# Optimization experiments

Hardware: AMD Instinct MI355X
Metric: run time of the kernel (lower is better)

The kernel has to match this reference:

```python
import jax, jax.numpy as jnp
import numpy as np

N_WIN, P, C = 2048, 64, 256      # total windows, tokens per window (8x8 partition), channels
M_SEL, KEEP, REAL = 1536, 48, 40 # selected windows, topk tokens kept per window, real (non-padded)
H, DH = 8, 32                    # heads, dim_head
EPS = 1e-5


def _ln(x, g, b):
    mu = jnp.mean(x, axis=-1, keepdims=True)
    v = jnp.mean(jnp.square(x - mu), axis=-1, keepdims=True)
    return (x - mu) * jax.lax.rsqrt(v + EPS) * g + b


def setup_inputs() -> dict:
    key = jax.random.key(0)
    ks = jax.random.split(key, 6)
    rng = np.random.default_rng(0)
    # distinct selected windows
    index_window = jnp.asarray(np.sort(rng.choice(N_WIN, size=M_SEL, replace=False)), jnp.int32)
    # per selected window: 48 distinct token positions out of 64; first 40 real, last 8 padded
    pos = np.argsort(rng.random((M_SEL, P)), axis=1)[:, :KEEP]
    tok = np.arange(M_SEL)[:, None] * P + pos           # flat rows into (M*P, C)
    index_token = jnp.asarray(tok.reshape(-1), jnp.int32)
    asy_index = jnp.asarray(tok[:, :REAL].reshape(-1), jnp.int32)
    padding_index = jnp.asarray(tok[:, REAL:].reshape(-1), jnp.int32)
    w = lambda k, s: jax.random.normal(k, s, jnp.float32) * 0.02
    return {
        "x": jax.random.normal(ks[0], (N_WIN, P, C), jnp.float32),
        "qkv_w": w(ks[1], (C, 3 * C)), "qkv_b": jnp.zeros((3 * C,), jnp.float32),
        "proj_w": w(ks[2], (C, C)), "proj_b": jnp.zeros((C,), jnp.float32),
        "norm1_g": jnp.ones((C,), jnp.float32), "norm1_b": jnp.zeros((C,), jnp.float32),
        "norm2_g": jnp.ones((C,), jnp.float32), "norm2_b": jnp.zeros((C,), jnp.float32),
        "ls1_g": jnp.full((C,), 1e-5, jnp.float32), "ls2_g": jnp.full((C,), 1e-5, jnp.float32),
        "mlp_w1": w(ks[3], (C, 4 * C)), "mlp_b1": jnp.zeros((4 * C,), jnp.float32),
        "mlp_w2": w(ks[4], (4 * C, C)), "mlp_b2": jnp.zeros((C,), jnp.float32),
        "index_window": index_window, "index_token": index_token,
        "padding_index": padding_index, "asy_index": asy_index,
        "M": M_SEL,
    }


def reference(x, qkv_w, qkv_b, proj_w, proj_b, norm1_g, norm1_b, norm2_g, norm2_b,
              ls1_g, ls2_g, mlp_w1, mlp_b1, mlp_w2, mlp_b2,
              index_window, index_token, padding_index, asy_index, M):
    scale = DH ** -0.5
    x1 = _ln(x, norm1_g, norm1_b)                       # norm1 over all windows (N,P,C)
    X = x1
    XX = x1[index_window].reshape(-1, C)                # gather selected windows -> (M*P, C)
    XX = XX.at[asy_index].set(_ln(XX[asy_index], norm2_g, norm2_b))
    shortcut = XX[asy_index]
    xt = XX[index_token].reshape(M, KEEP, C)            # gather kept tokens per window
    qkv = (xt @ qkv_w + qkv_b).reshape(M, KEEP, H, 3 * DH).transpose(0, 2, 1, 3)
    q, k, v = jnp.split(qkv, 3, axis=-1)                # each (M,H,KEEP,DH)
    attn = jnp.einsum('mhqd,mhkd->mhqk', q, k) * scale  # (M,H,Q,K)
    # scatter scores into full map keyed by KEY token row, mask padded keys, gather back
    am = attn.transpose(0, 3, 2, 1).reshape(M * KEEP, KEEP, H)
    attn_map = jnp.zeros((M * P, KEEP, H), attn.dtype)
    attn_map = attn_map.at[index_token].set(am)
    attn_map = attn_map.at[padding_index].set(-10000.0)
    attn = attn_map[index_token].reshape(M, KEEP, KEEP, H).transpose(0, 3, 2, 1)
    attn = jax.nn.softmax(attn, axis=-1)
    out = jnp.einsum('mhqk,mhkd->mhqd', attn, v).transpose(0, 2, 1, 3).reshape(M, KEEP, C)
    out = out @ proj_w + proj_b
    XX = XX.at[index_token].set(out.reshape(-1, C))
    xa = shortcut + XX[asy_index] * ls1_g               # residual + LayerScale
    hdn = jax.nn.gelu(xa @ mlp_w1 + mlp_b1, approximate=False)
    xa = xa + (hdn @ mlp_w2 + mlp_b2) * ls2_g           # (enable_CB=False path)
    XX = XX.at[asy_index].set(xa)
    Xw = X[index_window].reshape(-1, C)
    XX = XX.at[padding_index].set(Xw[padding_index])    # restore padded rows
    X = X.at[index_window].set(XX.reshape(M, P, C))     # scatter windows back
    return X
```

## Files before the change

### kernel.cpp

```cpp
#include <hip/hip_runtime.h>

typedef __attribute__((ext_vector_type(8))) short bf16x8;
typedef __attribute__((ext_vector_type(4))) float f32x4;
typedef unsigned short u16;
typedef unsigned int u32;

#define NWIN 2048
#define P 64
#define C 256
#define MSEL 1536
#define KEEP 48
#define REAL 40
#define H 8
#define DH 32
#define MROWS (MSEL * REAL)

#define OFF_WQKVT  0
#define OFF_PROJT  196608
#define OFF_W1T    262144
#define OFF_W2T    524288
#define OFF_A      786432
#define OFF_QKV    16515072
#define OFF_ATTNO  63700992
#define OFF_XA     79429632
#define OFF_H      16515072

__device__ __forceinline__ u16 f2bf(float f) {
    u32 u = __float_as_uint(f);
    u += 0x7FFF + ((u >> 16) & 1);
    return (u16)(u >> 16);
}
__device__ __forceinline__ float bf2f(u16 h) { return __uint_as_float(((u32)h) << 16); }

__global__ __launch_bounds__(256) void prep_weights(const float* __restrict__ qkv_w,
                                                    const float* __restrict__ proj_w,
                                                    const float* __restrict__ w1,
                                                    const float* __restrict__ w2,
                                                    u16* __restrict__ ws) {
    int i = blockIdx.x * 256 + threadIdx.x;
    float v; int o;
    if (i < 196608) {
        int n = i >> 8, k = i & 255; v = qkv_w[k * 768 + n]; o = OFF_WQKVT + i;
    } else if (i < 262144) {
        int j = i - 196608; int n = j >> 8, k = j & 255; v = proj_w[k * 256 + n]; o = i;
    } else if (i < 524288) {
        int j = i - 262144; int n = j >> 8, k = j & 255; v = w1[k * 1024 + n]; o = i;
    } else {
        int j = i - 524288; int n = j >> 10, k = j & 1023; v = w2[k * 256 + n]; o = i;
    }
    ws[o] = f2bf(v);
}

__global__ __launch_bounds__(256) void ln1_kernel(const float* __restrict__ x,
                                                  const float* __restrict__ g,
                                                  const float* __restrict__ b,
                                                  float* __restrict__ out) {
    int row = blockIdx.x * 4 + (threadIdx.x >> 6);
    int l = threadIdx.x & 63;
    const float4 v = *(const float4*)(x + (size_t)row * C + l * 4);
    float s = v.x + v.y + v.z + v.w;
    float q = v.x * v.x + v.y * v.y + v.z * v.z + v.w * v.w;
    #pragma unroll
    for (int m = 1; m < 64; m <<= 1) { s += __shfl_xor(s, m); q += __shfl_xor(q, m); }
    float mu = s * (1.0f / C);
    float var = q * (1.0f / C) - mu * mu;
    float rs = rsqrtf(var + 1e-5f);
    float4 gg = *(const float4*)(g + l * 4);
    float4 bb = *(const float4*)(b + l * 4);
    float4 o;
    o.x = (v.x - mu) * rs * gg.x + bb.x;
    o.y = (v.y - mu) * rs * gg.y + bb.y;
    o.z = (v.z - mu) * rs * gg.z + bb.z;
    o.w = (v.w - mu) * rs * gg.w + bb.w;
    *(float4*)(out + (size_t)row * C + l * 4) = o;
}

__global__ __launch_bounds__(256) void ln2_kernel(const float* __restrict__ ln1,
                                                  const float* __restrict__ g,
                                                  const float* __restrict__ b,
                                                  const int* __restrict__ asy,
                                                  const int* __restrict__ iwin,
                                                  u16* __restrict__ A) {
    int r = blockIdx.x * 4 + (threadIdx.x >> 6);
    int l = threadIdx.x & 63;
    int flat = asy[r];
    int m = flat >> 6, p = flat & 63;
    int w = iwin[m];
    const float4 v = *(const float4*)(ln1 + ((size_t)w * P + p) * C + l * 4);
    float s = v.x + v.y + v.z + v.w;
    float q = v.x * v.x + v.y * v.y + v.z * v.z + v.w * v.w;
    #pragma unroll
    for (int mm = 1; mm < 64; mm <<= 1) { s += __shfl_xor(s, mm); q += __shfl_xor(q, mm); }
    float mu = s * (1.0f / C);
    float var = q * (1.0f / C) - mu * mu;
    float rs = rsqrtf(var + 1e-5f);
    float4 gg = *(const float4*)(g + l * 4);
    float4 bb = *(const float4*)(b + l * 4);
    ushort4 o;
    o.x = f2bf((v.x - mu) * rs * gg.x + bb.x);
    o.y = f2bf((v.y - mu) * rs * gg.y + bb.y);
    o.z = f2bf((v.z - mu) * rs * gg.z + bb.z);
    o.w = f2bf((v.w - mu) * rs * gg.w + bb.w);
    *(ushort4*)(A + (size_t)r * C + l * 4) = o;
}

template <int N, int K, class Epi>
__global__ __launch_bounds__(256) void gemm_bt(const u16* __restrict__ A,
                                               const u16* __restrict__ B, Epi epi,
                                               int chunk) {
    constexpr int NB = N / 128;
    int bid = blockIdx.x;
    bid = (bid & 7) * chunk + (bid >> 3);
    int bm = bid / NB, bn = bid % NB;
    __shared__ u16 lA[128 * 64], lB[128 * 64];
    int t = threadIdx.x;
    int l = t & 63, w = t >> 6;
    int wr = w >> 1, wc = w & 1;
    int l15 = l & 15, g4 = l >> 4;
    int xr = l15 & 7;

    f32x4 acc[4][4];
    #pragma unroll
    for (int a = 0; a < 4; a++)
        #pragma unroll
        for (int bb = 0; bb < 4; bb++)
            #pragma unroll
            for (int i = 0; i < 4; i++) acc[a][bb][i] = 0.0f;

    int rbase = w * 32 + (l >> 3);
    int cg = (l & 7) ^ (l >> 3);
    const u16* gA = A + (size_t)(bm * 128 + rbase) * K + cg * 8;
    const u16* gB = B + (size_t)(bn * 128 + rbase) * K + cg * 8;

    for (int k0 = 0; k0 < K; k0 += 64) {
        __syncthreads();
        #pragma unroll
        for (int j = 0; j < 4; j++)
            __builtin_amdgcn_global_load_lds(
                (const __attribute__((address_space(1))) u32*)(gA + (size_t)j * 8 * K + k0),
                (__attribute__((address_space(3))) u32*)(lA + w * 2048 + j * 512), 16, 0, 0);
        #pragma unroll
        for (int j = 0; j < 4; j++)
            __builtin_amdgcn_global_load_lds(
                (const __attribute__((address_space(1))) u32*)(gB + (size_t)j * 8 * K + k0),
                (__attribute__((address_space(3))) u32*)(lB + w * 2048 + j * 512), 16, 0, 0);
        __syncthreads();
        #pragma unroll
        for (int kk = 0; kk < 2; kk++) {
            bf16x8 af[4], bfr[4];
            #pragma unroll
            for (int mt = 0; mt < 4; mt++)
                af[mt] = *(const bf16x8*)(lA + (wr * 64 + mt * 16 + l15) * 64
                                             + ((kk * 4 + g4) ^ xr) * 8);
            #pragma unroll
            for (int nt = 0; nt < 4; nt++)
                bfr[nt] = *(const bf16x8*)(lB + (wc * 64 + nt * 16 + l15) * 64
                                              + ((kk * 4 + g4) ^ xr) * 8);
            #pragma unroll
            for (int mt = 0; mt < 4; mt++)
                #pragma unroll
                for (int nt = 0; nt < 4; nt++)
                    acc[mt][nt] = __builtin_amdgcn_mfma_f32_16x16x32_bf16(af[mt], bfr[nt], acc[mt][nt], 0, 0, 0);
        }
    }
    int orow = bm * 128 + wr * 64, ocol = bn * 128 + wc * 64;
    #pragma unroll
    for (int mt = 0; mt < 4; mt++)
        #pragma unroll
        for (int nt = 0; nt < 4; nt++)
            #pragma unroll
            for (int rg = 0; rg < 4; rg++)
                epi(orow + mt * 16 + g4 * 4 + rg, ocol + nt * 16 + l15, acc[mt][nt][rg]);
}

struct EpiQKV {
    const float* bias; u16* out;
    __device__ void operator()(int r, int c, float v) const {
        out[(size_t)r * 768 + c] = f2bf(v + bias[c]);
    }
};
struct EpiProj {
    const float* bias; const float* ls1; const u16* Abuf; u16* xa;
    __device__ void operator()(int r, int c, float v) const {
        float val = bf2f(Abuf[(size_t)r * 256 + c]) + (v + bias[c]) * ls1[c];
        xa[(size_t)r * 256 + c] = f2bf(val);
    }
};
struct EpiMLP1 {
    const float* bias; u16* h;
    __device__ void operator()(int r, int c, float v) const {
        float x = v + bias[c];
        float gl = 0.5f * x * (1.0f + erff(x * 0.70710678118654752f));
        h[(size_t)r * 1024 + c] = f2bf(gl);
    }
};
struct EpiMLP2 {
    const float* bias; const float* ls2; const u16* xa;
    const int* asy; const int* iwin; float* out;
    __device__ void operator()(int r, int c, float v) const {
        float val = bf2f(xa[(size_t)r * 256 + c]) + (v + bias[c]) * ls2[c];
        int flat = asy[r];
        int m = flat >> 6, p = flat & 63;
        int wdw = iwin[m];
        out[((size_t)wdw * P + p) * C + c] = val;
    }
};

__global__ __launch_bounds__(256) void attn_kernel(const u16* __restrict__ QKV,
                                                   u16* __restrict__ out) {
    __shared__ u16 lds[4 * (48 * 80 + 32 * 80)];
    int m = blockIdx.x;
    int t = threadIdx.x, l = t & 63, w = t >> 6;
    int l15 = l & 15, g4 = l >> 4;
    u16* Pb = lds + w * (48 * 80 + 32 * 80);
    u16* Vt = Pb + 48 * 80;

    u32* z = (u32*)Pb;
    for (int i = l; i < (48 * 80 + 32 * 80) / 2; i += 64) z[i] = 0;

    const float scale = 0.17677669529663687f;

    for (int hh = 0; hh < 2; hh++) {
        int h = w + hh * 4;
        const u16* base = QKV + (size_t)m * REAL * 768 + h * 96;

        for (int i = l; i < REAL * 4; i += 64) {
            int kk = i >> 2, dg = i & 3;
            bf16x8 vv = *(const bf16x8*)(base + (size_t)kk * 768 + 64 + dg * 8);
            #pragma unroll
            for (int j = 0; j < 8; j++) Vt[(dg * 8 + j) * 80 + kk] = vv[j];
        }

        bf16x8 zf;
        #pragma unroll
        for (int i = 0; i < 8; i++) zf[i] = 0;
        bf16x8 qf[3], kf[3];
        #pragma unroll
        for (int mt = 0; mt < 3; mt++) {
            int q = mt * 16 + l15;
            qf[mt] = (q < REAL) ? *(const bf16x8*)(base + (size_t)q * 768 + g4 * 8) : zf;
        }
        #pragma unroll
        for (int nt = 0; nt < 3; nt++) {
            int kk = nt * 16 + l15;
            kf[nt] = (kk < REAL) ? *(const bf16x8*)(base + (size_t)kk * 768 + 32 + g4 * 8) : zf;
        }
        f32x4 s[3][3];
        #pragma unroll
        for (int a = 0; a < 3; a++)
            #pragma unroll
            for (int bb = 0; bb < 3; bb++)
                #pragma unroll
                for (int i = 0; i < 4; i++) s[a][bb][i] = 0.0f;
        #pragma unroll
        for (int mt = 0; mt < 3; mt++)
            #pragma unroll
            for (int nt = 0; nt < 3; nt++)
                s[mt][nt] = __builtin_amdgcn_mfma_f32_16x16x32_bf16(qf[mt], kf[nt], s[mt][nt], 0, 0, 0);

        #pragma unroll
        for (int mt = 0; mt < 3; mt++) {
            #pragma unroll
            for (int rg = 0; rg < 4; rg++) {
                float v0 = s[mt][0][rg] * scale;
                float v1 = s[mt][1][rg] * scale;
                float v2 = s[mt][2][rg] * scale;
                bool k2ok = (32 + l15) < REAL;
                float mx = fmaxf(fmaxf(v0, v1), k2ok ? v2 : -1e30f);
                #pragma unroll
                for (int xm = 1; xm < 16; xm <<= 1) mx = fmaxf(mx, __shfl_xor(mx, xm));
                float e0 = __expf(v0 - mx);
                float e1 = __expf(v1 - mx);
                float e2 = k2ok ? __expf(v2 - mx) : 0.0f;
                float sm = e0 + e1 + e2;
                #pragma unroll
                for (int xm = 1; xm < 16; xm <<= 1) sm += __shfl_xor(sm, xm);
                float inv = 1.0f / sm;
                int q = mt * 16 + g4 * 4 + rg;
                Pb[q * 80 + l15]      = f2bf(e0 * inv);
                Pb[q * 80 + 16 + l15] = f2bf(e1 * inv);
                Pb[q * 80 + 32 + l15] = f2bf(e2 * inv);
            }
        }

        f32x4 o[3][2];
        #pragma unroll
        for (int a = 0; a < 3; a++)
            #pragma unroll
            for (int bb = 0; bb < 2; bb++)
                #pragma unroll
                for (int i = 0; i < 4; i++) o[a][bb][i] = 0.0f;
        #pragma unroll
        for (int kt = 0; kt < 2; kt++) {
            bf16x8 pf[3], vf[2];
            #pragma unroll
            for (int mt = 0; mt < 3; mt++)
                pf[mt] = *(const bf16x8*)(Pb + (mt * 16 + l15) * 80 + kt * 32 + g4 * 8);
            #pragma unroll
            for (int nt = 0; nt < 2; nt++)
                vf[nt] = *(const bf16x8*)(Vt + (nt * 16 + l15) * 80 + kt * 32 + g4 * 8);
            #pragma unroll
            for (int mt = 0; mt < 3; mt++)
                #pragma unroll
                for (int nt = 0; nt < 2; nt++)
                    o[mt][nt] = __builtin_amdgcn_mfma_f32_16x16x32_bf16(pf[mt], vf[nt], o[mt][nt], 0, 0, 0);
        }
        #pragma unroll
        for (int mt = 0; mt < 3; mt++)
            #pragma unroll
            for (int nt = 0; nt < 2; nt++)
                #pragma unroll
                for (int rg = 0; rg < 4; rg++) {
                    int q = mt * 16 + g4 * 4 + rg;
                    if (q < REAL)
                        out[((size_t)m * REAL + q) * C + h * DH + nt * 16 + l15] = f2bf(o[mt][nt][rg]);
                }
    }
}

extern "C" void kernel_launch(void* const* d_in, const int* in_sizes, int n_in,
                              void* d_out, int out_size, void* d_ws, size_t ws_size,
                              hipStream_t stream) {
    const float* x      = (const float*)d_in[0];
    const float* qkv_w  = (const float*)d_in[1];
    const float* qkv_b  = (const float*)d_in[2];
    const float* proj_w = (const float*)d_in[3];
    const float* proj_b = (const float*)d_in[4];
    const float* n1g    = (const float*)d_in[5];
    const float* n1b    = (const float*)d_in[6];
    const float* n2g    = (const float*)d_in[7];
    const float* n2b    = (const float*)d_in[8];
    const float* ls1    = (const float*)d_in[9];
    const float* ls2    = (const float*)d_in[10];
    const float* w1     = (const float*)d_in[11];
    const float* b1     = (const float*)d_in[12];
    const float* w2     = (const float*)d_in[13];
    const float* b2     = (const float*)d_in[14];
    const int*   iwin   = (const int*)d_in[15];
    const int*   asy    = (const int*)d_in[18];
    float* out = (float*)d_out;
    u16* ws = (u16*)d_ws;

    u16* WqkvT = ws + OFF_WQKVT;
    u16* ProjT = ws + OFF_PROJT;
    u16* W1T   = ws + OFF_W1T;
    u16* W2T   = ws + OFF_W2T;
    u16* Abuf  = ws + OFF_A;
    u16* QKV   = ws + OFF_QKV;
    u16* AttnO = ws + OFF_ATTNO;
    u16* XA    = ws + OFF_XA;
    u16* Hbuf  = ws + OFF_H;

    prep_weights<<<3072, 256, 0, stream>>>(qkv_w, proj_w, w1, w2, ws);
    ln1_kernel<<<(NWIN * P) / 4, 256, 0, stream>>>(x, n1g, n1b, out);
    ln2_kernel<<<MROWS / 4, 256, 0, stream>>>(out, n2g, n2b, asy, iwin, Abuf);
    {
        int nwg = (MROWS / 128) * 6;
        gemm_bt<768, 256, EpiQKV><<<nwg, 256, 0, stream>>>(Abuf, WqkvT, EpiQKV{qkv_b, QKV}, nwg / 8);
    }
    attn_kernel<<<MSEL, 256, 0, stream>>>(QKV, AttnO);
    {
        int nwg = (MROWS / 128) * 2;
        gemm_bt<256, 256, EpiProj><<<nwg, 256, 0, stream>>>(AttnO, ProjT, EpiProj{proj_b, ls1, Abuf, XA}, nwg / 8);
    }
    {
        int nwg = (MROWS / 128) * 8;
        gemm_bt<1024, 256, EpiMLP1><<<nwg, 256, 0, stream>>>(XA, W1T, EpiMLP1{b1, Hbuf}, nwg / 8);
    }
    {
        int nwg = (MROWS / 128) * 2;
        gemm_bt<256, 1024, EpiMLP2><<<nwg, 256, 0, stream>>>(Hbuf, W2T, EpiMLP2{b2, ls2, XA, asy, iwin, out}, nwg / 8);
    }
}
```

Baseline: 517.7 us.

## Fuse proj, MLP1 with GELU, and MLP2 into one per-row-tile kernel

Replaces the three separate GEMM launches (projection, MLP up with GELU, MLP down) with one kernel that processes 64 rows per block. The projection output and the hidden activations stay in LDS, chunked 128 hidden columns at a time, so the XA and H intermediates never go to global memory. In exchange the weight B-fragments are read straight from global/L2 with no LDS staging or pipelining. The proj and MLP2 output tiles are smaller (64 rows) than the tuned 128x128 GEMM tiles, which may hurt MFMA efficiency.

```diff
diff --git a/kernel.cpp b/kernel.cpp
--- a/kernel.cpp
+++ b/kernel.cpp
@@ -22,8 +22,6 @@
 #define OFF_A      786432
 #define OFF_QKV    16515072
 #define OFF_ATTNO  63700992
-#define OFF_XA     79429632
-#define OFF_H      16515072
 
 __device__ __forceinline__ u16 f2bf(float f) {
     u32 u = __float_as_uint(f);
@@ -179,32 +177,6 @@
         out[(size_t)r * 768 + c] = f2bf(v + bias[c]);
     }
 };
-struct EpiProj {
-    const float* bias; const float* ls1; const u16* Abuf; u16* xa;
-    __device__ void operator()(int r, int c, float v) const {
-        float val = bf2f(Abuf[(size_t)r * 256 + c]) + (v + bias[c]) * ls1[c];
-        xa[(size_t)r * 256 + c] = f2bf(val);
-    }
-};
-struct EpiMLP1 {
-    const float* bias; u16* h;
-    __device__ void operator()(int r, int c, float v) const {
-        float x = v + bias[c];
-        float gl = 0.5f * x * (1.0f + erff(x * 0.70710678118654752f));
-        h[(size_t)r * 1024 + c] = f2bf(gl);
-    }
-};
-struct EpiMLP2 {
-    const float* bias; const float* ls2; const u16* xa;
-    const int* asy; const int* iwin; float* out;
-    __device__ void operator()(int r, int c, float v) const {
-        float val = bf2f(xa[(size_t)r * 256 + c]) + (v + bias[c]) * ls2[c];
-        int flat = asy[r];
-        int m = flat >> 6, p = flat & 63;
-        int wdw = iwin[m];
-        out[((size_t)wdw * P + p) * C + c] = val;
-    }
-};
 
 __global__ __launch_bounds__(256) void attn_kernel(const u16* __restrict__ QKV,
                                                    u16* __restrict__ out) {
@@ -316,6 +288,150 @@
                         out[((size_t)m * REAL + q) * C + h * DH + nt * 16 + l15] = f2bf(o[mt][nt][rg]);
                 }
     }
+}
+
+__global__ __launch_bounds__(256) void fused_tail(const u16* __restrict__ AttnO,
+                                                  const u16* __restrict__ Abuf,
+                                                  const u16* __restrict__ ProjT,
+                                                  const u16* __restrict__ W1T,
+                                                  const u16* __restrict__ W2T,
+                                                  const float* __restrict__ proj_b,
+                                                  const float* __restrict__ ls1,
+                                                  const float* __restrict__ b1,
+                                                  const float* __restrict__ b2,
+                                                  const float* __restrict__ ls2,
+                                                  const int* __restrict__ asy,
+                                                  const int* __restrict__ iwin,
+                                                  float* __restrict__ out) {
+    __shared__ u16 Xs[64 * 264];
+    __shared__ u16 Hs[64 * 136];
+    int r0 = blockIdx.x * 64;
+    int t = threadIdx.x, l = t & 63, w = t >> 6;
+    int l15 = l & 15, g4 = l >> 4;
+
+    #pragma unroll
+    for (int i = 0; i < 8; i++) {
+        int flat = i * 2048 + t * 8;
+        int row = flat >> 8, col = flat & 255;
+        bf16x8 v = *(const bf16x8*)(AttnO + (size_t)(r0 + row) * 256 + col);
+        *(bf16x8*)(Xs + row * 264 + col) = v;
+    }
+    __syncthreads();
+
+    f32x4 accp[4][4];
+    #pragma unroll
+    for (int a = 0; a < 4; a++)
+        #pragma unroll
+        for (int bb = 0; bb < 4; bb++)
+            #pragma unroll
+            for (int i = 0; i < 4; i++) accp[a][bb][i] = 0.0f;
+    for (int k0 = 0; k0 < 256; k0 += 32) {
+        bf16x8 af[4], bf[4];
+        #pragma unroll
+        for (int mt = 0; mt < 4; mt++)
+            af[mt] = *(const bf16x8*)(Xs + (mt * 16 + l15) * 264 + k0 + g4 * 8);
+        #pragma unroll
+        for (int nt = 0; nt < 4; nt++)
+            bf[nt] = *(const bf16x8*)(ProjT + (size_t)(w * 64 + nt * 16 + l15) * 256 + k0 + g4 * 8);
+        #pragma unroll
+        for (int mt = 0; mt < 4; mt++)
+            #pragma unroll
+            for (int nt = 0; nt < 4; nt++)
+                accp[mt][nt] = __builtin_amdgcn_mfma_f32_16x16x32_bf16(af[mt], bf[nt], accp[mt][nt], 0, 0, 0);
+    }
+    __syncthreads();
+
+    #pragma unroll
+    for (int nt = 0; nt < 4; nt++) {
+        int col = w * 64 + nt * 16 + l15;
+        float pb = proj_b[col], l1 = ls1[col];
+        #pragma unroll
+        for (int mt = 0; mt < 4; mt++)
+            #pragma unroll
+            for (int rg = 0; rg < 4; rg++) {
+                int row = mt * 16 + g4 * 4 + rg;
+                float xa = bf2f(Abuf[(size_t)(r0 + row) * 256 + col]) + (accp[mt][nt][rg] + pb) * l1;
+                Xs[row * 264 + col] = f2bf(xa);
+            }
+    }
+    __syncthreads();
+
+    f32x4 acco[4][4];
+    #pragma unroll
+    for (int a = 0; a < 4; a++)
+        #pragma unroll
+        for (int bb = 0; bb < 4; bb++)
+            #pragma unroll
+            for (int i = 0; i < 4; i++) acco[a][bb][i] = 0.0f;
+
+    for (int kc = 0; kc < 8; kc++) {
+        f32x4 acch[4][2];
+        #pragma unroll
+        for (int a = 0; a < 4; a++)
+            #pragma unroll
+            for (int bb = 0; bb < 2; bb++)
+                #pragma unroll
+                for (int i = 0; i < 4; i++) acch[a][bb][i] = 0.0f;
+        for (int k0 = 0; k0 < 256; k0 += 32) {
+            bf16x8 af[4], bf[2];
+            #pragma unroll
+            for (int mt = 0; mt < 4; mt++)
+                af[mt] = *(const bf16x8*)(Xs + (mt * 16 + l15) * 264 + k0 + g4 * 8);
+            #pragma unroll
+            for (int nt = 0; nt < 2; nt++)
+                bf[nt] = *(const bf16x8*)(W1T + (size_t)(kc * 128 + w * 32 + nt * 16 + l15) * 256 + k0 + g4 * 8);
+            #pragma unroll
+            for (int mt = 0; mt < 4; mt++)
+                #pragma unroll
+                for (int nt = 0; nt < 2; nt++)
+                    acch[mt][nt] = __builtin_amdgcn_mfma_f32_16x16x32_bf16(af[mt], bf[nt], acch[mt][nt], 0, 0, 0);
+        }
+        __syncthreads();
+        #pragma unroll
+        for (int nt = 0; nt < 2; nt++) {
+            int col = w * 32 + nt * 16 + l15;
+            float bb1 = b1[kc * 128 + col];
+            #pragma unroll
+            for (int mt = 0; mt < 4; mt++)
+                #pragma unroll
+                for (int rg = 0; rg < 4; rg++) {
+                    int row = mt * 16 + g4 * 4 + rg;
+                    float x = acch[mt][nt][rg] + bb1;
+                    float gl = 0.5f * x * (1.0f + erff(x * 0.70710678118654752f));
+                    Hs[row * 136 + col] = f2bf(gl);
+                }
+        }
+        __syncthreads();
+        for (int k0 = 0; k0 < 128; k0 += 32) {
+            bf16x8 af[4], bf[4];
+            #pragma unroll
+            for (int mt = 0; mt < 4; mt++)
+                af[mt] = *(const bf16x8*)(Hs + (mt * 16 + l15) * 136 + k0 + g4 * 8);
+            #pragma unroll
+            for (int nt = 0; nt < 4; nt++)
+                bf[nt] = *(const bf16x8*)(W2T + (size_t)(w * 64 + nt * 16 + l15) * 1024 + kc * 128 + k0 + g4 * 8);
+            #pragma unroll
+            for (int mt = 0; mt < 4; mt++)
+                #pragma unroll
+                for (int nt = 0; nt < 4; nt++)
+                    acco[mt][nt] = __builtin_amdgcn_mfma_f32_16x16x32_bf16(af[mt], bf[nt], acco[mt][nt], 0, 0, 0);
+        }
+    }
+
+    #pragma unroll
+    for (int mt = 0; mt < 4; mt++)
+        #pragma unroll
+        for (int rg = 0; rg < 4; rg++) {
+            int row = mt * 16 + g4 * 4 + rg;
+            int flat = asy[r0 + row];
+            size_t orow = ((size_t)iwin[flat >> 6] * P + (flat & 63)) * C;
+            #pragma unroll
+            for (int nt = 0; nt < 4; nt++) {
+                int col = w * 64 + nt * 16 + l15;
+                float xa = bf2f(Xs[row * 264 + col]);
+                out[orow + col] = xa + (acco[mt][nt][rg] + b2[col]) * ls2[col];
+            }
+        }
 }
 
 extern "C" void kernel_launch(void* const* d_in, const int* in_sizes, int n_in,
@@ -348,8 +464,6 @@
     u16* Abuf  = ws + OFF_A;
     u16* QKV   = ws + OFF_QKV;
     u16* AttnO = ws + OFF_ATTNO;
-    u16* XA    = ws + OFF_XA;
-    u16* Hbuf  = ws + OFF_H;
 
     prep_weights<<<3072, 256, 0, stream>>>(qkv_w, proj_w, w1, w2, ws);
     ln1_kernel<<<(NWIN * P) / 4, 256, 0, stream>>>(x, n1g, n1b, out);
@@ -359,16 +473,6 @@
         gemm_bt<768, 256, EpiQKV><<<nwg, 256, 0, stream>>>(Abuf, WqkvT, EpiQKV{qkv_b, QKV}, nwg / 8);
     }
     attn_kernel<<<MSEL, 256, 0, stream>>>(QKV, AttnO);
-    {
-        int nwg = (MROWS / 128) * 2;
-        gemm_bt<256, 256, EpiProj><<<nwg, 256, 0, stream>>>(AttnO, ProjT, EpiProj{proj_b, ls1, Abuf, XA}, nwg / 8);
-    }
-    {
-        int nwg = (MROWS / 128) * 8;
-        gemm_bt<1024, 256, EpiMLP1><<<nwg, 256, 0, stream>>>(XA, W1T, EpiMLP1{b1, Hbuf}, nwg / 8);
-    }
-    {
-        int nwg = (MROWS / 128) * 2;
-        gemm_bt<256, 1024, EpiMLP2><<<nwg, 256, 0, stream>>>(Hbuf, W2T, EpiMLP2{b2, ls2, XA, asy, iwin, out}, nwg / 8);
-    }
-}
+    fused_tail<<<MROWS / 64, 256, 0, stream>>>(AttnO, Abuf, ProjT, W1T, W2T,
+                                               proj_b, ls1, b1, b2, ls2, asy, iwin, out);
+}
```

After: 561.3 us. +8.4%, slower.
